# Performance work log

Hardware: AMD Instinct MI355X
Metric: run time of the kernel (lower is better)

Reference implementation:

```python
import jax, jax.numpy as jnp
import numpy as np

B, N, FIN, H, D = 2, 512, 128, 4, 64
NEG_SLOPE = 0.2


def setup_inputs() -> dict:
    key = jax.random.key(0)
    ks = jax.random.split(key, 5)
    x = jax.random.normal(ks[0], (B, N, FIN), dtype=jnp.float32)
    # xavier-ish scaled params
    W_proj = jax.random.normal(ks[1], (H, FIN, D), dtype=jnp.float32) * (1.0 / np.sqrt(FIN + D))
    b_proj = jnp.zeros((H, D), dtype=jnp.float32)
    W_cat_weight = jax.random.normal(ks[2], (H, D, 2 * D), dtype=jnp.float32) * (1.0 / np.sqrt(3 * D))
    W_cat_bias = jnp.zeros((H, D), dtype=jnp.float32)
    a = jax.random.normal(ks[3], (H, D), dtype=jnp.float32) * (1.0 / np.sqrt(D))
    bias_param = jnp.zeros((H * D,), dtype=jnp.float32)
    return {"x": x, "W_proj": W_proj, "b_proj": b_proj,
            "W_cat_weight": W_cat_weight, "W_cat_bias": W_cat_bias,
            "a": a, "bias_param": bias_param}


def reference(x, W_proj, b_proj, W_cat_weight, W_cat_bias, a, bias_param):
    # h[b,h,n,d] = W^h x_n + b^h
    h = jnp.einsum('bni,hid->bhnd', x, W_proj) + b_proj[None, :, None, :]
    d = h.shape[-1]
    # W_cat [h_i || h_j] == W1 h_i + W2 h_j  (avoids O(N^2*2D) concat tensor)
    W1 = W_cat_weight[:, :, :d]   # (H, D, D) acts on source node i
    W2 = W_cat_weight[:, :, d:]   # (H, D, D) acts on target node j
    zi = jnp.einsum('bhnd,hed->bhne', h, W1)  # (B,H,N,D)
    zj = jnp.einsum('bhnd,hed->bhne', h, W2)  # (B,H,N,D)
    # z[b,h,i,j,e] = zi[b,h,i,e] + zj[b,h,j,e] + bias, then LeakyReLU
    z = zi[:, :, :, None, :] + zj[:, :, None, :, :] + W_cat_bias[None, :, None, None, :]
    z = jnp.where(z >= 0, z, NEG_SLOPE * z)
    # e[b,h,i,j] = a_h . z
    e = jnp.einsum('bhije,he->bhij', z, a)
    attn = jax.nn.softmax(e, axis=-1)          # softmax over neighbors j
    out = jnp.einsum('bhij,bhjd->bhid', attn, h)  # (B,H,N,D)
    b_, h_, n_, d_ = out.shape
    out = out.transpose(0, 2, 1, 3).reshape(b_, n_, h_ * d_)  # concat heads
    out = out + bias_param
    return out
```

## Files before the change

kernel.cpp:

```cpp
#include <hip/hip_runtime.h>
#include <hip/hip_bf16.h>

#define BB 2
#define NN 512
#define FIN 128
#define HH 4
#define DD 64


__global__ __launch_bounds__(256) void proj_kernel(
    const float* __restrict__ x, const float* __restrict__ Wp,
    const float* __restrict__ bp, const float* __restrict__ Wc,
    const float* __restrict__ Wcb, const float* __restrict__ a,
    float* __restrict__ h_ws, float* __restrict__ zi_ws, float* __restrict__ zj_ws,
    float* __restrict__ adi_ws, float* __restrict__ adj_ws)
{
    int blk = blockIdx.x;
    int bh = blk >> 6;
    int n0 = (blk & 63) << 3;
    int b = bh >> 2, hh = bh & 3;

    __shared__ float xs[8 * FIN];
    __shared__ float hs[8][DD];
    __shared__ float Wcs[DD][2 * DD + 1];

    int t = threadIdx.x;

    ((float4*)xs)[t] = ((const float4*)(x + ((size_t)b * NN + n0) * FIN))[t];
    {
        const float4* wg = (const float4*)(Wc + (size_t)hh * DD * 2 * DD);
        #pragma unroll
        for (int k = 0; k < 8; ++k) {
            int idx = t + 256 * k;
            int r = idx >> 5, c4 = (idx & 31) * 4;
            float4 v = wg[idx];
            Wcs[r][c4] = v.x; Wcs[r][c4 + 1] = v.y;
            Wcs[r][c4 + 2] = v.z; Wcs[r][c4 + 3] = v.w;
        }
    }
    __syncthreads();

    int d = t & 63, w = t >> 6;
    const float* Wph = Wp + (size_t)hh * FIN * DD;
    float bpv = bp[hh * DD + d];
    float acc0 = bpv, acc1 = bpv;
    #pragma unroll 8
    for (int i = 0; i < FIN; ++i) {
        float wv = Wph[i * DD + d];
        acc0 = fmaf(xs[w * FIN + i], wv, acc0);
        acc1 = fmaf(xs[(w + 4) * FIN + i], wv, acc1);
    }
    hs[w][d] = acc0; hs[w + 4][d] = acc1;
    float* hg = h_ws + ((size_t)bh * NN + n0) * DD;
    hg[w * DD + d] = acc0; hg[(w + 4) * DD + d] = acc1;
    __syncthreads();

    int e = d;
    float zb = Wcb[hh * DD + e];
    float zi0 = zb, zi1 = zb, zj0 = 0.f, zj1 = 0.f;
    #pragma unroll 8
    for (int d2 = 0; d2 < DD; ++d2) {
        float w1 = Wcs[e][d2];
        float w2 = Wcs[e][DD + d2];
        float h0 = hs[w][d2], h1 = hs[w + 4][d2];
        zi0 = fmaf(h0, w1, zi0); zi1 = fmaf(h1, w1, zi1);
        zj0 = fmaf(h0, w2, zj0); zj1 = fmaf(h1, w2, zj1);
    }
    float* zib = zi_ws + ((size_t)bh * NN + n0) * DD;
    float* zjb = zj_ws + ((size_t)bh * NN + n0) * DD;
    zib[w * DD + e] = zi0; zib[(w + 4) * DD + e] = zi1;
    zjb[w * DD + e] = zj0; zjb[(w + 4) * DD + e] = zj1;

    float av = a[hh * DD + e];
    float p0 = av * zi0, p1 = av * zi1, q0 = av * zj0, q1 = av * zj1;
    #pragma unroll
    for (int off = 32; off; off >>= 1) {
        p0 += __shfl_xor(p0, off); p1 += __shfl_xor(p1, off);
        q0 += __shfl_xor(q0, off); q1 += __shfl_xor(q1, off);
    }
    if (e == 0) {
        adi_ws[bh * NN + n0 + w]     = 0.6f * p0;
        adi_ws[bh * NN + n0 + w + 4] = 0.6f * p1;
        adj_ws[bh * NN + n0 + w]     = 0.6f * q0;
        adj_ws[bh * NN + n0 + w + 4] = 0.6f * q1;
    }
}

__global__ __launch_bounds__(256) void attn_kernel(
    const float* __restrict__ h_ws, const float* __restrict__ zi_ws,
    const float* __restrict__ zj_ws, const float* __restrict__ a,
    const float* __restrict__ adi_ws, const float* __restrict__ adj_ws,
    float* __restrict__ pacc, float* __restrict__ pm, float* __restrict__ ps)
{
    int blk = blockIdx.x;
    int js = blk & 1;
    int it = (blk >> 1) & 63;
    int bh = blk >> 7;
    int i0 = it << 3;
    int hh = bh & 3;

    __shared__ float zis[8][DD];
    __shared__ float as[DD];
    __shared__ float adis[8];
    __shared__ float tile[64][65];
    __shared__ float es[8][256];
    __shared__ float pms[8], pss[8];

    int t = threadIdx.x;
    int jl = t & 63, g = t >> 6;
    int r0 = 2 * g, r1 = 2 * g + 1;

    if (t < 128) ((float4*)zis)[t] =
        ((const float4*)(zi_ws + ((size_t)bh * NN + i0) * DD))[t];
    if (t < DD) as[t] = 0.4f * a[hh * DD + t];
    if (t < 8)  adis[t] = adi_ws[bh * NN + i0 + t];

    const float* zjb  = zj_ws + ((size_t)bh * NN + js * 256) * DD;
    const float* hb   = h_ws  + ((size_t)bh * NN + js * 256) * DD;
    const float* adjb = adj_ws + bh * NN + js * 256;

    for (int jt = 0; jt < 4; ++jt) {
        __syncthreads();
        const float4* src = (const float4*)(zjb + (size_t)jt * 64 * DD);
        #pragma unroll
        for (int k = 0; k < 4; ++k) {
            int idx = t + 256 * k, r = idx >> 4, c4 = (idx & 15) * 4;
            float4 v = src[idx];
            tile[r][c4] = v.x; tile[r][c4 + 1] = v.y;
            tile[r][c4 + 2] = v.z; tile[r][c4 + 3] = v.w;
        }
        float adjv = adjb[jt * 64 + jl];
        __syncthreads();

        float acc0 = 0.f, acc1 = 0.f;
        const float4* z0p = (const float4*)zis[r0];
        const float4* z1p = (const float4*)zis[r1];
        const float4* a4p = (const float4*)as;
        const float*  trow = tile[jl];
        #pragma unroll
        for (int e4 = 0; e4 < 16; ++e4) {
            float4 za = z0p[e4], zb4 = z1p[e4], av = a4p[e4];
            float t0 = trow[4 * e4 + 0];
            float t1 = trow[4 * e4 + 1];
            float t2 = trow[4 * e4 + 2];
            float t3 = trow[4 * e4 + 3];
            acc0 = fmaf(av.x, __builtin_fabsf(za.x + t0), acc0);
            acc0 = fmaf(av.y, __builtin_fabsf(za.y + t1), acc0);
            acc0 = fmaf(av.z, __builtin_fabsf(za.z + t2), acc0);
            acc0 = fmaf(av.w, __builtin_fabsf(za.w + t3), acc0);
            acc1 = fmaf(av.x, __builtin_fabsf(zb4.x + t0), acc1);
            acc1 = fmaf(av.y, __builtin_fabsf(zb4.y + t1), acc1);
            acc1 = fmaf(av.z, __builtin_fabsf(zb4.z + t2), acc1);
            acc1 = fmaf(av.w, __builtin_fabsf(zb4.w + t3), acc1);
        }
        es[r0][jt * 64 + jl] = adis[r0] + adjv + acc0;
        es[r1][jt * 64 + jl] = adis[r1] + adjv + acc1;
    }
    __syncthreads();

    {
        int r = t >> 5, l = t & 31;
        float m = -1e30f;
        #pragma unroll
        for (int k = 0; k < 8; ++k) m = fmaxf(m, es[r][l + 32 * k]);
        #pragma unroll
        for (int off = 16; off; off >>= 1) m = fmaxf(m, __shfl_xor(m, off));
        float s = 0.f;
        #pragma unroll
        for (int k = 0; k < 8; ++k) {
            float p = __expf(es[r][l + 32 * k] - m);
            es[r][l + 32 * k] = p;
            s += p;
        }
        #pragma unroll
        for (int off = 16; off; off >>= 1) s += __shfl_xor(s, off);
        if (l == 0) { pms[r] = m; pss[r] = s; }
    }

    float acc0 = 0.f, acc1 = 0.f;
    for (int jt = 0; jt < 4; ++jt) {
        __syncthreads();
        const float4* src = (const float4*)(hb + (size_t)jt * 64 * DD);
        #pragma unroll
        for (int k = 0; k < 4; ++k) {
            int idx = t + 256 * k, r = idx >> 4, c4 = (idx & 15) * 4;
            float4 v = src[idx];
            tile[r][c4] = v.x; tile[r][c4 + 1] = v.y;
            tile[r][c4 + 2] = v.z; tile[r][c4 + 3] = v.w;
        }
        __syncthreads();
        const float4* e0p = (const float4*)&es[r0][jt * 64];
        const float4* e1p = (const float4*)&es[r1][jt * 64];
        #pragma unroll
        for (int j4 = 0; j4 < 16; ++j4) {
            float4 p0 = e0p[j4], p1 = e1p[j4];
            float h0 = tile[4 * j4 + 0][jl];
            float h1 = tile[4 * j4 + 1][jl];
            float h2 = tile[4 * j4 + 2][jl];
            float h3 = tile[4 * j4 + 3][jl];
            acc0 = fmaf(p0.x, h0, acc0); acc1 = fmaf(p1.x, h0, acc1);
            acc0 = fmaf(p0.y, h1, acc0); acc1 = fmaf(p1.y, h1, acc1);
            acc0 = fmaf(p0.z, h2, acc0); acc1 = fmaf(p1.z, h2, acc1);
            acc0 = fmaf(p0.w, h3, acc0); acc1 = fmaf(p1.w, h3, acc1);
        }
    }

    size_t rowbase = ((size_t)js * 8 + bh) * NN;
    pacc[(rowbase + i0 + r0) * DD + jl] = acc0;
    pacc[(rowbase + i0 + r1) * DD + jl] = acc1;
    if (t < 8) {
        pm[js * 4096 + bh * NN + i0 + t] = pms[t];
        ps[js * 4096 + bh * NN + i0 + t] = pss[t];
    }
}

__global__ __launch_bounds__(256) void combine_kernel(
    const float* __restrict__ pacc, const float* __restrict__ pm,
    const float* __restrict__ ps, const float* __restrict__ bias_param,
    float* __restrict__ out)
{
    int tid = blockIdx.x * 256 + threadIdx.x;
    int d = tid & 63;
    int row = tid >> 6;
    int bh = row >> 9, n = row & 511;
    int b = bh >> 2, hh = bh & 3;
    float m0 = pm[row], m1 = pm[4096 + row];
    float s0 = ps[row], s1 = ps[4096 + row];
    float M = fmaxf(m0, m1);
    float w0 = __expf(m0 - M), w1 = __expf(m1 - M);
    float inv = 1.f / fmaf(s0, w0, s1 * w1);
    float a0 = pacc[(size_t)row * 64 + d];
    float a1 = pacc[262144 + (size_t)row * 64 + d];
    out[((size_t)b * NN + n) * (HH * DD) + hh * DD + d] =
        fmaf(a0, w0, a1 * w1) * inv + bias_param[hh * DD + d];
}

extern "C" void kernel_launch(void* const* d_in, const int* in_sizes, int n_in,
                              void* d_out, int out_size, void* d_ws, size_t ws_size,
                              hipStream_t stream) {
    const float* x    = (const float*)d_in[0];
    const float* Wp   = (const float*)d_in[1];
    const float* bp   = (const float*)d_in[2];
    const float* Wc   = (const float*)d_in[3];
    const float* Wcb  = (const float*)d_in[4];
    const float* a    = (const float*)d_in[5];
    const float* bpar = (const float*)d_in[6];
    float* out = (float*)d_out;

    float* ws    = (float*)d_ws;
    float* h_ws   = ws;
    float* zi_ws  = ws + 262144;
    float* zj_ws  = ws + 524288;
    float* adi_ws = ws + 786432;
    float* adj_ws = ws + 790528;
    float* pacc   = ws + 794624;
    float* pm     = ws + 1318912;
    float* ps     = ws + 1327104;

    proj_kernel<<<dim3(512), dim3(256), 0, stream>>>(
        x, Wp, bp, Wc, Wcb, a, h_ws, zi_ws, zj_ws, adi_ws, adj_ws);
    attn_kernel<<<dim3(1024), dim3(256), 0, stream>>>(
        h_ws, zi_ws, zj_ws, a, adi_ws, adj_ws, pacc, pm, ps);
    combine_kernel<<<dim3(1024), dim3(256), 0, stream>>>(
        pacc, pm, ps, bpar, out);
}
```

Before: 46.82 us.

## Retile attention into 16-row by 128-column blocks with 4-way split-K softmax

The attention kernel now gives each block 16 query rows and a quarter of the key range instead of 8 rows and half. Each wave computes 4 rows per thread, with zi and a read straight from global memory in uniform, broadcast-style loads. Scores are stored transposed so one float4 LDS read feeds four accumulators in the PV loop. The combine kernel now merges four partial softmax results instead of two. This raises register reuse per LDS load and keeps 1024 blocks, at the cost of more partial-result traffic and a larger workspace.

```diff
diff --git a/kernel.cpp b/kernel.cpp
--- a/kernel.cpp
+++ b/kernel.cpp
@@ -93,33 +93,36 @@
     float* __restrict__ pacc, float* __restrict__ pm, float* __restrict__ ps)
 {
     int blk = blockIdx.x;
-    int js = blk & 1;
-    int it = (blk >> 1) & 63;
+    int js = blk & 3;
+    int it = (blk >> 2) & 31;
     int bh = blk >> 7;
-    int i0 = it << 3;
+    int i0 = it << 4;
     int hh = bh & 3;
 
-    __shared__ float zis[8][DD];
-    __shared__ float as[DD];
-    __shared__ float adis[8];
-    __shared__ float tile[64][65];
-    __shared__ float es[8][256];
-    __shared__ float pms[8], pss[8];
+    __shared__ float tile[64][68];
+    __shared__ float esT[128][20];
+    __shared__ float pms[16], pss[16];
 
     int t = threadIdx.x;
-    int jl = t & 63, g = t >> 6;
-    int r0 = 2 * g, r1 = 2 * g + 1;
-
-    if (t < 128) ((float4*)zis)[t] =
-        ((const float4*)(zi_ws + ((size_t)bh * NN + i0) * DD))[t];
-    if (t < DD) as[t] = 0.4f * a[hh * DD + t];
-    if (t < 8)  adis[t] = adi_ws[bh * NN + i0 + t];
-
-    const float* zjb  = zj_ws + ((size_t)bh * NN + js * 256) * DD;
-    const float* hb   = h_ws  + ((size_t)bh * NN + js * 256) * DD;
-    const float* adjb = adj_ws + bh * NN + js * 256;
-
-    for (int jt = 0; jt < 4; ++jt) {
+    int jl = t & 63;
+    int w  = __builtin_amdgcn_readfirstlane(t >> 6);
+    int r0 = i0 + 4 * w;
+
+    const float4* zi0 = (const float4*)(zi_ws + ((size_t)bh * NN + r0 + 0) * DD);
+    const float4* zi1 = (const float4*)(zi_ws + ((size_t)bh * NN + r0 + 1) * DD);
+    const float4* zi2 = (const float4*)(zi_ws + ((size_t)bh * NN + r0 + 2) * DD);
+    const float4* zi3 = (const float4*)(zi_ws + ((size_t)bh * NN + r0 + 3) * DD);
+    const float4* a4  = (const float4*)(a + hh * DD);
+    float adi0 = adi_ws[bh * NN + r0 + 0];
+    float adi1 = adi_ws[bh * NN + r0 + 1];
+    float adi2 = adi_ws[bh * NN + r0 + 2];
+    float adi3 = adi_ws[bh * NN + r0 + 3];
+
+    const float* zjb  = zj_ws + ((size_t)bh * NN + js * 128) * DD;
+    const float* hb   = h_ws  + ((size_t)bh * NN + js * 128) * DD;
+    const float* adjb = adj_ws + bh * NN + js * 128;
+
+    for (int jt = 0; jt < 2; ++jt) {
         __syncthreads();
         const float4* src = (const float4*)(zjb + (size_t)jt * 64 * DD);
         #pragma unroll
@@ -132,53 +135,61 @@
         float adjv = adjb[jt * 64 + jl];
         __syncthreads();
 
-        float acc0 = 0.f, acc1 = 0.f;
-        const float4* z0p = (const float4*)zis[r0];
-        const float4* z1p = (const float4*)zis[r1];
-        const float4* a4p = (const float4*)as;
-        const float*  trow = tile[jl];
+        float acc0 = 0.f, acc1 = 0.f, acc2 = 0.f, acc3 = 0.f;
+        const float4* trow = (const float4*)tile[jl];
         #pragma unroll
         for (int e4 = 0; e4 < 16; ++e4) {
-            float4 za = z0p[e4], zb4 = z1p[e4], av = a4p[e4];
-            float t0 = trow[4 * e4 + 0];
-            float t1 = trow[4 * e4 + 1];
-            float t2 = trow[4 * e4 + 2];
-            float t3 = trow[4 * e4 + 3];
-            acc0 = fmaf(av.x, __builtin_fabsf(za.x + t0), acc0);
-            acc0 = fmaf(av.y, __builtin_fabsf(za.y + t1), acc0);
-            acc0 = fmaf(av.z, __builtin_fabsf(za.z + t2), acc0);
-            acc0 = fmaf(av.w, __builtin_fabsf(za.w + t3), acc0);
-            acc1 = fmaf(av.x, __builtin_fabsf(zb4.x + t0), acc1);
-            acc1 = fmaf(av.y, __builtin_fabsf(zb4.y + t1), acc1);
-            acc1 = fmaf(av.z, __builtin_fabsf(zb4.z + t2), acc1);
-            acc1 = fmaf(av.w, __builtin_fabsf(zb4.w + t3), acc1);
-        }
-        es[r0][jt * 64 + jl] = adis[r0] + adjv + acc0;
-        es[r1][jt * 64 + jl] = adis[r1] + adjv + acc1;
+            float4 tv = trow[e4];
+            float4 av = a4[e4];
+            float4 z0 = zi0[e4], z1 = zi1[e4];
+            float4 z2 = zi2[e4], z3 = zi3[e4];
+            acc0 = fmaf(av.x, __builtin_fabsf(z0.x + tv.x), acc0);
+            acc0 = fmaf(av.y, __builtin_fabsf(z0.y + tv.y), acc0);
+            acc0 = fmaf(av.z, __builtin_fabsf(z0.z + tv.z), acc0);
+            acc0 = fmaf(av.w, __builtin_fabsf(z0.w + tv.w), acc0);
+            acc1 = fmaf(av.x, __builtin_fabsf(z1.x + tv.x), acc1);
+            acc1 = fmaf(av.y, __builtin_fabsf(z1.y + tv.y), acc1);
+            acc1 = fmaf(av.z, __builtin_fabsf(z1.z + tv.z), acc1);
+            acc1 = fmaf(av.w, __builtin_fabsf(z1.w + tv.w), acc1);
+            acc2 = fmaf(av.x, __builtin_fabsf(z2.x + tv.x), acc2);
+            acc2 = fmaf(av.y, __builtin_fabsf(z2.y + tv.y), acc2);
+            acc2 = fmaf(av.z, __builtin_fabsf(z2.z + tv.z), acc2);
+            acc2 = fmaf(av.w, __builtin_fabsf(z2.w + tv.w), acc2);
+            acc3 = fmaf(av.x, __builtin_fabsf(z3.x + tv.x), acc3);
+            acc3 = fmaf(av.y, __builtin_fabsf(z3.y + tv.y), acc3);
+            acc3 = fmaf(av.z, __builtin_fabsf(z3.z + tv.z), acc3);
+            acc3 = fmaf(av.w, __builtin_fabsf(z3.w + tv.w), acc3);
+        }
+        float4 es4;
+        es4.x = adi0 + adjv + 0.4f * acc0;
+        es4.y = adi1 + adjv + 0.4f * acc1;
+        es4.z = adi2 + adjv + 0.4f * acc2;
+        es4.w = adi3 + adjv + 0.4f * acc3;
+        *(float4*)&esT[jt * 64 + jl][4 * w] = es4;
     }
     __syncthreads();
 
     {
-        int r = t >> 5, l = t & 31;
+        int r = t >> 4, l = t & 15;
         float m = -1e30f;
         #pragma unroll
-        for (int k = 0; k < 8; ++k) m = fmaxf(m, es[r][l + 32 * k]);
-        #pragma unroll
-        for (int off = 16; off; off >>= 1) m = fmaxf(m, __shfl_xor(m, off));
+        for (int k = 0; k < 8; ++k) m = fmaxf(m, esT[l + 16 * k][r]);
+        #pragma unroll
+        for (int off = 8; off; off >>= 1) m = fmaxf(m, __shfl_xor(m, off));
         float s = 0.f;
         #pragma unroll
         for (int k = 0; k < 8; ++k) {
-            float p = __expf(es[r][l + 32 * k] - m);
-            es[r][l + 32 * k] = p;
+            float p = __expf(esT[l + 16 * k][r] - m);
+            esT[l + 16 * k][r] = p;
             s += p;
         }
         #pragma unroll
-        for (int off = 16; off; off >>= 1) s += __shfl_xor(s, off);
+        for (int off = 8; off; off >>= 1) s += __shfl_xor(s, off);
         if (l == 0) { pms[r] = m; pss[r] = s; }
     }
 
-    float acc0 = 0.f, acc1 = 0.f;
-    for (int jt = 0; jt < 4; ++jt) {
+    float acc0 = 0.f, acc1 = 0.f, acc2 = 0.f, acc3 = 0.f;
+    for (int jt = 0; jt < 2; ++jt) {
         __syncthreads();
         const float4* src = (const float4*)(hb + (size_t)jt * 64 * DD);
         #pragma unroll
@@ -189,28 +200,25 @@
             tile[r][c4 + 2] = v.z; tile[r][c4 + 3] = v.w;
         }
         __syncthreads();
-        const float4* e0p = (const float4*)&es[r0][jt * 64];
-        const float4* e1p = (const float4*)&es[r1][jt * 64];
-        #pragma unroll
-        for (int j4 = 0; j4 < 16; ++j4) {
-            float4 p0 = e0p[j4], p1 = e1p[j4];
-            float h0 = tile[4 * j4 + 0][jl];
-            float h1 = tile[4 * j4 + 1][jl];
-            float h2 = tile[4 * j4 + 2][jl];
-            float h3 = tile[4 * j4 + 3][jl];
-            acc0 = fmaf(p0.x, h0, acc0); acc1 = fmaf(p1.x, h0, acc1);
-            acc0 = fmaf(p0.y, h1, acc0); acc1 = fmaf(p1.y, h1, acc1);
-            acc0 = fmaf(p0.z, h2, acc0); acc1 = fmaf(p1.z, h2, acc1);
-            acc0 = fmaf(p0.w, h3, acc0); acc1 = fmaf(p1.w, h3, acc1);
-        }
-    }
-
-    size_t rowbase = ((size_t)js * 8 + bh) * NN;
-    pacc[(rowbase + i0 + r0) * DD + jl] = acc0;
-    pacc[(rowbase + i0 + r1) * DD + jl] = acc1;
-    if (t < 8) {
-        pm[js * 4096 + bh * NN + i0 + t] = pms[t];
-        ps[js * 4096 + bh * NN + i0 + t] = pss[t];
+        #pragma unroll 16
+        for (int j = 0; j < 64; ++j) {
+            float4 p = *(const float4*)&esT[jt * 64 + j][4 * w];
+            float hv = tile[j][jl];
+            acc0 = fmaf(p.x, hv, acc0);
+            acc1 = fmaf(p.y, hv, acc1);
+            acc2 = fmaf(p.z, hv, acc2);
+            acc3 = fmaf(p.w, hv, acc3);
+        }
+    }
+
+    size_t rowbase = ((size_t)(js * 8 + bh) * NN + r0);
+    pacc[(rowbase + 0) * DD + jl] = acc0;
+    pacc[(rowbase + 1) * DD + jl] = acc1;
+    pacc[(rowbase + 2) * DD + jl] = acc2;
+    pacc[(rowbase + 3) * DD + jl] = acc3;
+    if (t < 16) {
+        pm[(js * 8 + bh) * NN + i0 + t] = pms[t];
+        ps[(js * 8 + bh) * NN + i0 + t] = pss[t];
     }
 }
 
@@ -224,15 +232,19 @@
     int row = tid >> 6;
     int bh = row >> 9, n = row & 511;
     int b = bh >> 2, hh = bh & 3;
-    float m0 = pm[row], m1 = pm[4096 + row];
-    float s0 = ps[row], s1 = ps[4096 + row];
-    float M = fmaxf(m0, m1);
+    float m0 = pm[row],         m1 = pm[4096 + row];
+    float m2 = pm[8192 + row],  m3 = pm[12288 + row];
+    float M = fmaxf(fmaxf(m0, m1), fmaxf(m2, m3));
     float w0 = __expf(m0 - M), w1 = __expf(m1 - M);
-    float inv = 1.f / fmaf(s0, w0, s1 * w1);
-    float a0 = pacc[(size_t)row * 64 + d];
-    float a1 = pacc[262144 + (size_t)row * 64 + d];
+    float w2 = __expf(m2 - M), w3 = __expf(m3 - M);
+    float denom = ps[row] * w0 + ps[4096 + row] * w1
+                + ps[8192 + row] * w2 + ps[12288 + row] * w3;
+    float acc = pacc[(size_t)row * 64 + d] * w0
+              + pacc[262144 + (size_t)row * 64 + d] * w1
+              + pacc[524288 + (size_t)row * 64 + d] * w2
+              + pacc[786432 + (size_t)row * 64 + d] * w3;
     out[((size_t)b * NN + n) * (HH * DD) + hh * DD + d] =
-        fmaf(a0, w0, a1 * w1) * inv + bias_param[hh * DD + d];
+        acc / denom + bias_param[hh * DD + d];
 }
 
 extern "C" void kernel_launch(void* const* d_in, const int* in_sizes, int n_in,
@@ -247,15 +259,15 @@
     const float* bpar = (const float*)d_in[6];
     float* out = (float*)d_out;
 
-    float* ws    = (float*)d_ws;
+    float* ws     = (float*)d_ws;
     float* h_ws   = ws;
     float* zi_ws  = ws + 262144;
     float* zj_ws  = ws + 524288;
     float* adi_ws = ws + 786432;
     float* adj_ws = ws + 790528;
     float* pacc   = ws + 794624;
-    float* pm     = ws + 1318912;
-    float* ps     = ws + 1327104;
+    float* pm     = ws + 1843200;
+    float* ps     = ws + 1859584;
 
     proj_kernel<<<dim3(512), dim3(256), 0, stream>>>(
         x, Wp, bp, Wc, Wcb, a, h_ws, zi_ws, zj_ws, adi_ws, adj_ws);
```

Result: slower. 48.93 us (+4.5%).

## Fold attention vector into z by sign-grouped permutation and retile attention into 64x64 blocks

Applied to the files above, without the earlier changes.

A new prep kernel sorts the attention vector entries by sign and stores permuted absolute values. The projection kernel then writes zi and zj pre-scaled by |a| in that permuted, padded order, so the score loop needs only one uniform sign per float4 group instead of a per-element multiply by a. The attention kernel now tiles 64 queries by 64 keys per block, holding zj and h rows in registers and doing the softmax per row with wave shuffles. This gives 8 key splits, which the combine kernel merges. The aim is to cut ALU work and LDS traffic in the score loop, at the cost of more register pressure, a larger partial buffer and one extra tiny launch.

```diff
diff --git a/kernel.cpp b/kernel.cpp
--- a/kernel.cpp
+++ b/kernel.cpp
@@ -1,18 +1,38 @@
 #include <hip/hip_runtime.h>
 #include <hip/hip_bf16.h>
 
-#define BB 2
 #define NN 512
 #define FIN 128
 #define HH 4
 #define DD 64
-
+#define SW 68
+
+
+__global__ void prep_kernel(const float* __restrict__ a, float* __restrict__ sgn,
+                            float* __restrict__ pa, int* __restrict__ src)
+{
+    int h = threadIdx.x;
+    if (h >= HH) return;
+    const float* ah = a + h * DD;
+    int np = 0;
+    for (int e = 0; e < DD; ++e) if (ah[e] >= 0.f) ++np;
+    int GP = (np + 3) >> 2;
+    for (int s = 0; s < SW; ++s) { src[h*SW+s] = 0; pa[h*SW+s] = 0.f; }
+    int ip = 0, in_ = 4 * GP;
+    for (int e = 0; e < DD; ++e) {
+        float v = ah[e];
+        int s = (v >= 0.f) ? (ip++) : (in_++);
+        src[h*SW+s] = e; pa[h*SW+s] = fabsf(v);
+    }
+    for (int g = 0; g < 17; ++g) sgn[h*17+g] = (g < GP) ? 0.4f : -0.4f;
+}
 
 __global__ __launch_bounds__(256) void proj_kernel(
     const float* __restrict__ x, const float* __restrict__ Wp,
     const float* __restrict__ bp, const float* __restrict__ Wc,
     const float* __restrict__ Wcb, const float* __restrict__ a,
-    float* __restrict__ h_ws, float* __restrict__ zi_ws, float* __restrict__ zj_ws,
+    const float* __restrict__ pa_ws, const int* __restrict__ src_ws,
+    float* __restrict__ h_ws, float* __restrict__ azi_ws, float* __restrict__ azj_ws,
     float* __restrict__ adi_ws, float* __restrict__ adj_ws)
 {
     int blk = blockIdx.x;
@@ -23,6 +43,8 @@
     __shared__ float xs[8 * FIN];
     __shared__ float hs[8][DD];
     __shared__ float Wcs[DD][2 * DD + 1];
+    __shared__ float tzi[8][DD];
+    __shared__ float tzj[8][DD];
 
     int t = threadIdx.x;
 
@@ -66,10 +88,8 @@
         zi0 = fmaf(h0, w1, zi0); zi1 = fmaf(h1, w1, zi1);
         zj0 = fmaf(h0, w2, zj0); zj1 = fmaf(h1, w2, zj1);
     }
-    float* zib = zi_ws + ((size_t)bh * NN + n0) * DD;
-    float* zjb = zj_ws + ((size_t)bh * NN + n0) * DD;
-    zib[w * DD + e] = zi0; zib[(w + 4) * DD + e] = zi1;
-    zjb[w * DD + e] = zj0; zjb[(w + 4) * DD + e] = zj1;
+    tzi[w][e] = zi0; tzi[w + 4][e] = zi1;
+    tzj[w][e] = zj0; tzj[w + 4][e] = zj1;
 
     float av = a[hh * DD + e];
     float p0 = av * zi0, p1 = av * zi1, q0 = av * zj0, q1 = av * zj1;
@@ -84,133 +104,119 @@
         adj_ws[bh * NN + n0 + w]     = 0.6f * q0;
         adj_ws[bh * NN + n0 + w + 4] = 0.6f * q1;
     }
+    __syncthreads();
+
+    {
+        int r = t >> 5, sl = t & 31;
+        const int*   sh = src_ws + hh * SW;
+        const float* ph = pa_ws + hh * SW;
+        float* azib = azi_ws + ((size_t)bh * NN + n0) * SW;
+        float* azjb = azj_ws + ((size_t)bh * NN + n0) * SW;
+        for (int s = sl; s < SW; s += 32) {
+            int se = sh[s]; float pav = ph[s];
+            azib[(size_t)r * SW + s] = pav * tzi[r][se];
+            azjb[(size_t)r * SW + s] = pav * tzj[r][se];
+        }
+    }
 }
 
 __global__ __launch_bounds__(256) void attn_kernel(
-    const float* __restrict__ h_ws, const float* __restrict__ zi_ws,
-    const float* __restrict__ zj_ws, const float* __restrict__ a,
-    const float* __restrict__ adi_ws, const float* __restrict__ adj_ws,
+    const float* __restrict__ h_ws, const float* __restrict__ azi_ws,
+    const float* __restrict__ azj_ws, const float* __restrict__ adi_ws,
+    const float* __restrict__ adj_ws, const float* __restrict__ sgn_ws,
     float* __restrict__ pacc, float* __restrict__ pm, float* __restrict__ ps)
 {
     int blk = blockIdx.x;
-    int js = blk & 1;
-    int it = (blk >> 1) & 63;
-    int bh = blk >> 7;
-    int i0 = it << 3;
-    int hh = bh & 3;
-
-    __shared__ float zis[8][DD];
-    __shared__ float as[DD];
-    __shared__ float adis[8];
-    __shared__ float tile[64][65];
-    __shared__ float es[8][256];
-    __shared__ float pms[8], pss[8];
-
-    int t = threadIdx.x;
-    int jl = t & 63, g = t >> 6;
-    int r0 = 2 * g, r1 = 2 * g + 1;
-
-    if (t < 128) ((float4*)zis)[t] =
-        ((const float4*)(zi_ws + ((size_t)bh * NN + i0) * DD))[t];
-    if (t < DD) as[t] = 0.4f * a[hh * DD + t];
-    if (t < 8)  adis[t] = adi_ws[bh * NN + i0 + t];
-
-    const float* zjb  = zj_ws + ((size_t)bh * NN + js * 256) * DD;
-    const float* hb   = h_ws  + ((size_t)bh * NN + js * 256) * DD;
-    const float* adjb = adj_ws + bh * NN + js * 256;
-
-    for (int jt = 0; jt < 4; ++jt) {
-        __syncthreads();
-        const float4* src = (const float4*)(zjb + (size_t)jt * 64 * DD);
-        #pragma unroll
-        for (int k = 0; k < 4; ++k) {
-            int idx = t + 256 * k, r = idx >> 4, c4 = (idx & 15) * 4;
-            float4 v = src[idx];
-            tile[r][c4] = v.x; tile[r][c4 + 1] = v.y;
-            tile[r][c4 + 2] = v.z; tile[r][c4 + 3] = v.w;
-        }
-        float adjv = adjb[jt * 64 + jl];
-        __syncthreads();
-
+    int js = blk & 7, it = (blk >> 3) & 7, bh = blk >> 6;
+    int j0 = js << 6, i0 = it << 6, hh = bh & 3;
+
+    __shared__ float azis[64 * SW];
+    __shared__ float buf[64][SW];
+
+    int t = threadIdx.x, lane = t & 63;
+    int w = __builtin_amdgcn_readfirstlane(t >> 6);
+
+    {
+        const float4* srcp = (const float4*)(azi_ws + ((size_t)bh * NN + i0) * SW);
+        float4* dst = (float4*)azis;
+        #pragma unroll
+        for (int k = 0; k < 5; ++k) {
+            int idx = t + 256 * k;
+            if (idx < 64 * SW / 4) dst[idx] = srcp[idx];
+        }
+    }
+
+    float4 azj[17];
+    {
+        const float4* src4 = (const float4*)(azj_ws + ((size_t)bh * NN + j0 + lane) * SW);
+        #pragma unroll
+        for (int k = 0; k < 17; ++k) azj[k] = src4[k];
+    }
+    float adjv = adj_ws[bh * NN + j0 + lane];
+    float sgn[17];
+    {
+        const float* sg = sgn_ws + hh * 17;
+        #pragma unroll
+        for (int k = 0; k < 17; ++k) sgn[k] = sg[k];
+    }
+    const float* adib = adi_ws + bh * NN + i0;
+
+    __syncthreads();
+
+    float pmk = 0.f, psk = 0.f;
+    #pragma unroll 2
+    for (int ii = 0; ii < 16; ++ii) {
+        int i = 16 * w + ii;
+        const float4* arow = (const float4*)(azis + i * SW);
         float acc0 = 0.f, acc1 = 0.f;
-        const float4* z0p = (const float4*)zis[r0];
-        const float4* z1p = (const float4*)zis[r1];
-        const float4* a4p = (const float4*)as;
-        const float*  trow = tile[jl];
-        #pragma unroll
-        for (int e4 = 0; e4 < 16; ++e4) {
-            float4 za = z0p[e4], zb4 = z1p[e4], av = a4p[e4];
-            float t0 = trow[4 * e4 + 0];
-            float t1 = trow[4 * e4 + 1];
-            float t2 = trow[4 * e4 + 2];
-            float t3 = trow[4 * e4 + 3];
-            acc0 = fmaf(av.x, __builtin_fabsf(za.x + t0), acc0);
-            acc0 = fmaf(av.y, __builtin_fabsf(za.y + t1), acc0);
-            acc0 = fmaf(av.z, __builtin_fabsf(za.z + t2), acc0);
-            acc0 = fmaf(av.w, __builtin_fabsf(za.w + t3), acc0);
-            acc1 = fmaf(av.x, __builtin_fabsf(zb4.x + t0), acc1);
-            acc1 = fmaf(av.y, __builtin_fabsf(zb4.y + t1), acc1);
-            acc1 = fmaf(av.z, __builtin_fabsf(zb4.z + t2), acc1);
-            acc1 = fmaf(av.w, __builtin_fabsf(zb4.w + t3), acc1);
-        }
-        es[r0][jt * 64 + jl] = adis[r0] + adjv + acc0;
-        es[r1][jt * 64 + jl] = adis[r1] + adjv + acc1;
-    }
-    __syncthreads();
-
-    {
-        int r = t >> 5, l = t & 31;
-        float m = -1e30f;
-        #pragma unroll
-        for (int k = 0; k < 8; ++k) m = fmaxf(m, es[r][l + 32 * k]);
-        #pragma unroll
-        for (int off = 16; off; off >>= 1) m = fmaxf(m, __shfl_xor(m, off));
-        float s = 0.f;
-        #pragma unroll
-        for (int k = 0; k < 8; ++k) {
-            float p = __expf(es[r][l + 32 * k] - m);
-            es[r][l + 32 * k] = p;
-            s += p;
-        }
-        #pragma unroll
-        for (int off = 16; off; off >>= 1) s += __shfl_xor(s, off);
-        if (l == 0) { pms[r] = m; pss[r] = s; }
-    }
-
-    float acc0 = 0.f, acc1 = 0.f;
-    for (int jt = 0; jt < 4; ++jt) {
-        __syncthreads();
-        const float4* src = (const float4*)(hb + (size_t)jt * 64 * DD);
-        #pragma unroll
-        for (int k = 0; k < 4; ++k) {
-            int idx = t + 256 * k, r = idx >> 4, c4 = (idx & 15) * 4;
-            float4 v = src[idx];
-            tile[r][c4] = v.x; tile[r][c4 + 1] = v.y;
-            tile[r][c4 + 2] = v.z; tile[r][c4 + 3] = v.w;
-        }
-        __syncthreads();
-        const float4* e0p = (const float4*)&es[r0][jt * 64];
-        const float4* e1p = (const float4*)&es[r1][jt * 64];
-        #pragma unroll
-        for (int j4 = 0; j4 < 16; ++j4) {
-            float4 p0 = e0p[j4], p1 = e1p[j4];
-            float h0 = tile[4 * j4 + 0][jl];
-            float h1 = tile[4 * j4 + 1][jl];
-            float h2 = tile[4 * j4 + 2][jl];
-            float h3 = tile[4 * j4 + 3][jl];
-            acc0 = fmaf(p0.x, h0, acc0); acc1 = fmaf(p1.x, h0, acc1);
-            acc0 = fmaf(p0.y, h1, acc0); acc1 = fmaf(p1.y, h1, acc1);
-            acc0 = fmaf(p0.z, h2, acc0); acc1 = fmaf(p1.z, h2, acc1);
-            acc0 = fmaf(p0.w, h3, acc0); acc1 = fmaf(p1.w, h3, acc1);
-        }
-    }
-
-    size_t rowbase = ((size_t)js * 8 + bh) * NN;
-    pacc[(rowbase + i0 + r0) * DD + jl] = acc0;
-    pacc[(rowbase + i0 + r1) * DD + jl] = acc1;
-    if (t < 8) {
-        pm[js * 4096 + bh * NN + i0 + t] = pms[t];
-        ps[js * 4096 + bh * NN + i0 + t] = pss[t];
+        #pragma unroll
+        for (int k = 0; k < 17; ++k) {
+            float4 zi4 = arow[k];
+            float s = sgn[k];
+            acc0 = fmaf(s, __builtin_fabsf(zi4.x + azj[k].x), acc0);
+            acc1 = fmaf(s, __builtin_fabsf(zi4.y + azj[k].y), acc1);
+            acc0 = fmaf(s, __builtin_fabsf(zi4.z + azj[k].z), acc0);
+            acc1 = fmaf(s, __builtin_fabsf(zi4.w + azj[k].w), acc1);
+        }
+        float e = adib[i] + adjv + acc0 + acc1;
+        float m = e;
+        #pragma unroll
+        for (int off = 32; off; off >>= 1) m = fmaxf(m, __shfl_xor(m, off));
+        float p = __expf(e - m);
+        float ssum = p;
+        #pragma unroll
+        for (int off = 32; off; off >>= 1) ssum += __shfl_xor(ssum, off);
+        buf[i][lane] = p;
+        pmk = (lane == ii) ? m : pmk;
+        psk = (lane == ii) ? ssum : psk;
+    }
+
+    float hreg[64];
+    {
+        const float* hb = h_ws + ((size_t)bh * NN + j0) * DD + lane;
+        #pragma unroll
+        for (int j = 0; j < 64; ++j) hreg[j] = hb[j * DD];
+    }
+
+    size_t obase = ((size_t)(js * 8 + bh) * NN + i0) * DD + lane;
+    #pragma unroll 2
+    for (int ii = 0; ii < 16; ++ii) {
+        int i = 16 * w + ii;
+        const float4* prow = (const float4*)buf[i];
+        float a0 = 0.f, a1 = 0.f;
+        #pragma unroll
+        for (int k = 0; k < 16; ++k) {
+            float4 p4 = prow[k];
+            a0 = fmaf(p4.x, hreg[4 * k + 0], a0);
+            a1 = fmaf(p4.y, hreg[4 * k + 1], a1);
+            a0 = fmaf(p4.z, hreg[4 * k + 2], a0);
+            a1 = fmaf(p4.w, hreg[4 * k + 3], a1);
+        }
+        pacc[obase + (size_t)i * DD] = a0 + a1;
+    }
+    if (lane < 16) {
+        int r = (js * 8 + bh) * NN + i0 + 16 * w + lane;
+        pm[r] = pmk; ps[r] = psk;
     }
 }
 
@@ -224,15 +230,19 @@
     int row = tid >> 6;
     int bh = row >> 9, n = row & 511;
     int b = bh >> 2, hh = bh & 3;
-    float m0 = pm[row], m1 = pm[4096 + row];
-    float s0 = ps[row], s1 = ps[4096 + row];
-    float M = fmaxf(m0, m1);
-    float w0 = __expf(m0 - M), w1 = __expf(m1 - M);
-    float inv = 1.f / fmaf(s0, w0, s1 * w1);
-    float a0 = pacc[(size_t)row * 64 + d];
-    float a1 = pacc[262144 + (size_t)row * 64 + d];
+    float mv[8];
+    float m = -1e30f;
+    #pragma unroll
+    for (int p = 0; p < 8; ++p) { mv[p] = pm[p * 4096 + row]; m = fmaxf(m, mv[p]); }
+    float denom = 0.f, acc = 0.f;
+    #pragma unroll
+    for (int p = 0; p < 8; ++p) {
+        float wgt = __expf(mv[p] - m);
+        denom = fmaf(ps[p * 4096 + row], wgt, denom);
+        acc = fmaf(pacc[(size_t)p * 262144 + (size_t)row * 64 + d], wgt, acc);
+    }
     out[((size_t)b * NN + n) * (HH * DD) + hh * DD + d] =
-        fmaf(a0, w0, a1 * w1) * inv + bias_param[hh * DD + d];
+        acc / denom + bias_param[hh * DD + d];
 }
 
 extern "C" void kernel_launch(void* const* d_in, const int* in_sizes, int n_in,
@@ -247,20 +257,25 @@
     const float* bpar = (const float*)d_in[6];
     float* out = (float*)d_out;
 
-    float* ws    = (float*)d_ws;
+    float* ws     = (float*)d_ws;
     float* h_ws   = ws;
-    float* zi_ws  = ws + 262144;
-    float* zj_ws  = ws + 524288;
-    float* adi_ws = ws + 786432;
-    float* adj_ws = ws + 790528;
-    float* pacc   = ws + 794624;
-    float* pm     = ws + 1318912;
-    float* ps     = ws + 1327104;
-
+    float* azi_ws = ws + 262144;
+    float* azj_ws = ws + 540672;
+    float* adi_ws = ws + 819200;
+    float* adj_ws = ws + 823296;
+    float* pacc   = ws + 827392;
+    float* pm     = ws + 2924544;
+    float* ps     = ws + 2957312;
+    float* sgn_ws = ws + 2990080;
+    float* pa_ws  = ws + 2990148;
+    int*   src_ws = (int*)(ws + 2990420);
+
+    prep_kernel<<<dim3(1), dim3(64), 0, stream>>>(a, sgn_ws, pa_ws, src_ws);
     proj_kernel<<<dim3(512), dim3(256), 0, stream>>>(
-        x, Wp, bp, Wc, Wcb, a, h_ws, zi_ws, zj_ws, adi_ws, adj_ws);
-    attn_kernel<<<dim3(1024), dim3(256), 0, stream>>>(
-        h_ws, zi_ws, zj_ws, a, adi_ws, adj_ws, pacc, pm, ps);
+        x, Wp, bp, Wc, Wcb, a, pa_ws, src_ws,
+        h_ws, azi_ws, azj_ws, adi_ws, adj_ws);
+    attn_kernel<<<dim3(512), dim3(256), 0, stream>>>(
+        h_ws, azi_ws, azj_ws, adi_ws, adj_ws, sgn_ws, pacc, pm, ps);
     combine_kernel<<<dim3(1024), dim3(256), 0, stream>>>(
         pacc, pm, ps, bpar, out);
 }
```

Result: slower. 50.18 us (+7.2%).
